# Performance work log

Measured on AMD Instinct MI355X. Metric: run time of the kernel, lower is better.

## Reference

```python
import jax, jax.numpy as jnp
import numpy as np

B, T, D = 1024, 20, 50          # batch sessions, seq len (hardcoded 20), emb dim (hardcoded 50)
S1S2 = 50 * 20                  # sample1 * sample2 friend nodes (GAT src)
DEG = 50                        # avg in-degree per dst node
E = B * DEG
NUM_USERS, NUM_ITEMS = 100000, 50000


def _lstm(x, W_ih, W_hh, b_ih, b_hh):
    """PyTorch-style LSTM (gate order i,f,g,o). x: [N,T,D] -> hs: [T,N,D]."""
    N = x.shape[0]
    h0 = jnp.zeros((N, x.shape[-1]), x.dtype)
    def step(carry, xt):
        h, c = carry
        gates = xt @ W_ih.T + h @ W_hh.T + b_ih + b_hh
        i, f, g, o = jnp.split(gates, 4, axis=-1)
        c = jax.nn.sigmoid(f) * c + jax.nn.sigmoid(i) * jnp.tanh(g)
        h = jax.nn.sigmoid(o) * jnp.tanh(c)
        return (h, c), h
    (_, _), hs = jax.lax.scan(step, (h0, h0), jnp.swapaxes(x, 0, 1))
    return hs


def _gat(feat_src, feat_dst, edge_src, edge_dst, fc_W, fc_b):
    """u_dot_v -> edge_softmax (per dst) -> u_mul_e_sum -> relu(fc)."""
    n_dst = feat_dst.shape[0]
    src_e = feat_src[edge_src]                           # [E, D] gather
    score = jnp.sum(src_e * feat_dst[edge_dst], axis=-1) # [E] u_dot_v
    m = jax.ops.segment_max(score, edge_dst, num_segments=n_dst)
    ex = jnp.exp(score - m[edge_dst])
    den = jax.ops.segment_sum(ex, edge_dst, num_segments=n_dst)
    w = ex / den[edge_dst]                               # edge_softmax
    agg = jax.ops.segment_sum(w[:, None] * src_e, edge_dst, num_segments=n_dst)
    return jax.nn.relu(agg @ fc_W.T + fc_b)


def setup_inputs() -> dict:
    key = jax.random.key(0)
    ks = jax.random.split(key, 16)
    input_session = jax.random.randint(ks[0], (B, T), 0, NUM_ITEMS, dtype=jnp.int32)
    support_nodes_layer1 = jax.random.randint(ks[1], (S1S2,), 0, NUM_USERS, dtype=jnp.int32)
    support_sessions_layer1 = jax.random.randint(ks[2], (S1S2, T), 0, NUM_ITEMS, dtype=jnp.int32)
    edge_src = jax.random.randint(ks[3], (E,), 0, S1S2, dtype=jnp.int32)
    edge_dst = jnp.repeat(jnp.arange(B, dtype=jnp.int32), DEG)  # every dst has DEG edges
    s = 0.05
    user_emb = jax.random.normal(ks[4], (NUM_USERS, D), jnp.float32) * s
    item_emb = (jax.random.normal(ks[5], (NUM_ITEMS, D), jnp.float32) * s).at[0].set(0.0)  # padding_idx=0
    W_ih = jax.random.normal(ks[6], (4 * D, D), jnp.float32) * s
    W_hh = jax.random.normal(ks[7], (4 * D, D), jnp.float32) * s
    b_ih = jax.random.normal(ks[8], (4 * D,), jnp.float32) * s
    b_hh = jax.random.normal(ks[9], (4 * D,), jnp.float32) * s
    W1 = jax.random.normal(ks[10], (D, 2 * D), jnp.float32) * s
    fc_W = jax.random.normal(ks[11], (D, D), jnp.float32) * s
    fc_b = jax.random.normal(ks[12], (D,), jnp.float32) * s
    W2 = jax.random.normal(ks[13], (D, 3 * D), jnp.float32) * s
    return {"input_session": input_session, "support_nodes_layer1": support_nodes_layer1,
            "support_sessions_layer1": support_sessions_layer1, "edge_src": edge_src,
            "edge_dst": edge_dst, "user_emb": user_emb, "item_emb": item_emb,
            "W_ih": W_ih, "W_hh": W_hh, "b_ih": b_ih, "b_hh": b_hh,
            "W1": W1, "fc_W": fc_W, "fc_b": fc_b, "W2": W2}


def reference(input_session, support_nodes_layer1, support_sessions_layer1, edge_src, edge_dst,
              user_emb, item_emb, W_ih, W_hh, b_ih, b_hh, W1, fc_W, fc_b, W2):
    # current-user short-term: LSTM over session item embeddings, take last hidden
    output = _lstm(item_emb[input_session], W_ih, W_hh, b_ih, b_hh)[-1]        # [B, D]
    # friends long-term (user emb) + short-term (LSTM over friend sessions, step 0 as in source)
    long_term1 = user_emb[support_nodes_layer1]                                 # [S1S2, D]
    short_term1 = _lstm(item_emb[support_sessions_layer1], W_ih, W_hh, b_ih, b_hh)[0]  # [S1S2, D]
    ls1 = jax.nn.relu(jnp.concatenate([long_term1, short_term1], axis=-1) @ W1.T)      # [S1S2, D]
    # GAT: gather -> per-dst edge softmax -> scatter weighted sum
    gat_out = _gat(ls1, output, edge_src, edge_dst, fc_W, fc_b)                 # [B, D]
    feat = jnp.concatenate([output, gat_out], axis=-1)                          # [B, 2D]
    sr = jnp.concatenate([output, feat], axis=-1) @ W2.T                        # [B, D]
    logits = sr @ item_emb[1:].T                                                # [B, NUM_ITEMS-1]
    return logits
```

## Files before the change

### kernel.cpp

```cpp
#include <hip/hip_runtime.h>
#include <math.h>

#define D 50
#define T 20
#define BATCH 1024
#define S1S2 1000
#define DEG 50
#define NITEMS 50000
#define NLOGITS 49999
#define KPAD 64
#define SLAB 16
#define GROUPS 8
#define GSPAN 6400
#define ITERW 256
#define NITER 25
#define NIPAD 51200
#define LSTR2 276
#define PREP_BLKS ((NIPAD * (KPAD / 2) + 255) / 256)

using bf16x8 = __attribute__((ext_vector_type(8))) __bf16;
using f32x4  = __attribute__((ext_vector_type(4))) float;

__device__ __forceinline__ float sigf(float x) { return 1.0f / (1.0f + expf(-x)); }

__device__ __forceinline__ unsigned short f2bf(float f) {
    unsigned u = __builtin_bit_cast(unsigned, f);
    u = (u + 0x7FFFu + ((u >> 16) & 1u)) >> 16;
    return (unsigned short)u;
}

__global__ __launch_bounds__(256) void fused_front_kernel(
    const int* __restrict__ sess,
    const int* __restrict__ nodes,
    const int* __restrict__ fsess,
    const float* __restrict__ user_emb,
    const float* __restrict__ item_emb,
    const float* __restrict__ W_ih,
    const float* __restrict__ W_hh,
    const float* __restrict__ b_ih,
    const float* __restrict__ b_hh,
    const float* __restrict__ W1,
    float* __restrict__ out_h,
    float* __restrict__ ls1,
    unsigned* __restrict__ item_u)
{
    const int blk = blockIdx.x;
    const int t = threadIdx.x;

    if (blk < BATCH) {
        const int b = blk;
        __shared__ float x_s[D];
        __shared__ float h_s[D];
        __shared__ float g_s[4 * D];
        __shared__ int idx_s[T];

        if (t < T) idx_s[t] = sess[b * T + t];

        float wih[D], whh[D];
        float bias = 0.f;
        if (t < 4 * D) {
            #pragma unroll
            for (int k = 0; k < D; ++k) {
                wih[k] = W_ih[t * D + k];
                whh[k] = W_hh[t * D + k];
            }
            bias = b_ih[t] + b_hh[t];
        }
        float c = 0.f;
        if (t < D) h_s[t] = 0.f;
        __syncthreads();
        if (t < D) x_s[t] = item_emb[(size_t)idx_s[0] * D + t];
        __syncthreads();

        for (int step = 0; step < T; ++step) {
            float xn = 0.f;
            if (t < D && step + 1 < T)
                xn = item_emb[(size_t)idx_s[step + 1] * D + t];
            if (t < 4 * D) {
                float g = bias;
                #pragma unroll
                for (int k = 0; k < D; ++k)
                    g += wih[k] * x_s[k] + whh[k] * h_s[k];
                g_s[t] = g;
            }
            __syncthreads();
            if (t < D) {
                float ig = sigf(g_s[t]);
                float fg = sigf(g_s[D + t]);
                float gg = tanhf(g_s[2 * D + t]);
                float og = sigf(g_s[3 * D + t]);
                c = fg * c + ig * gg;
                h_s[t] = og * tanhf(c);
                if (step + 1 < T) x_s[t] = xn;
            }
            __syncthreads();
        }
        if (t < D) out_h[b * D + t] = h_s[t];
    } else if (blk < BATCH + S1S2) {
        const int s = blk - BATCH;
        __shared__ float fx_s[D];
        __shared__ float fh_s[D];
        __shared__ float fg_s[4 * D];

        if (t < D) fx_s[t] = item_emb[(size_t)fsess[s * T] * D + t];
        __syncthreads();
        if (t < 4 * D) {
            float g = b_ih[t] + b_hh[t];
            #pragma unroll
            for (int k = 0; k < D; ++k) g += W_ih[t * D + k] * fx_s[k];
            fg_s[t] = g;
        }
        __syncthreads();
        if (t < D) {
            float ig = sigf(fg_s[t]);
            float gg = tanhf(fg_s[2 * D + t]);
            float og = sigf(fg_s[3 * D + t]);
            float c1 = ig * gg;
            fh_s[t] = og * tanhf(c1);
        }
        __syncthreads();
        if (t < D) {
            const int node = nodes[s];
            const float* ue = user_emb + (size_t)node * D;
            const float* w1r = W1 + t * 2 * D;
            float acc = 0.f;
            #pragma unroll
            for (int k = 0; k < D; ++k) acc += ue[k] * w1r[k];
            #pragma unroll
            for (int k = 0; k < D; ++k) acc += fh_s[k] * w1r[D + k];
            ls1[s * D + t] = fmaxf(acc, 0.f);
        }
    } else {
        const int idx = (blk - BATCH - S1S2) * 256 + t;
        if (idx >= NIPAD * (KPAD / 2)) return;
        const int r = idx >> 5, c2 = idx & 31;
        const int c0 = c2 * 2, c1 = c0 + 1;
        float f0 = 0.f, f1 = 0.f;
        if (r < NLOGITS) {
            const float* row = item_emb + (size_t)(1 + r) * D;
            if (c0 < D) f0 = row[c0];
            if (c1 < D) f1 = row[c1];
        }
        item_u[idx] = (unsigned)f2bf(f0) | ((unsigned)f2bf(f1) << 16);
    }
}

__global__ __launch_bounds__(64) void gat_sr_kernel(
    const float* __restrict__ out_h,
    const float* __restrict__ ls1,
    const int* __restrict__ edge_src,
    const float* __restrict__ fc_W,
    const float* __restrict__ fc_b,
    const float* __restrict__ W2,
    unsigned* __restrict__ sr_u)
{
    const int b = blockIdx.x;
    const int l = threadIdx.x;
    __shared__ float q[D];
    __shared__ int srcs[DEG];
    __shared__ float w_s[DEG];
    __shared__ float a_s[D];
    __shared__ float g_s[D];
    __shared__ float srow_s[KPAD];

    srow_s[l] = 0.f;
    if (l < D) q[l] = out_h[b * D + l];
    if (l < DEG) srcs[l] = edge_src[b * DEG + l];
    __syncthreads();

    float sc = -INFINITY;
    if (l < DEG) {
        const float* row = ls1 + (size_t)srcs[l] * D;
        float s = 0.f;
        #pragma unroll
        for (int k = 0; k < D; ++k) s += row[k] * q[k];
        sc = s;
    }
    float m = sc;
    #pragma unroll
    for (int off = 32; off; off >>= 1) m = fmaxf(m, __shfl_xor(m, off));
    float ex = (l < DEG) ? expf(sc - m) : 0.f;
    float den = ex;
    #pragma unroll
    for (int off = 32; off; off >>= 1) den += __shfl_xor(den, off);
    if (l < DEG) w_s[l] = ex / den;
    __syncthreads();

    if (l < D) {
        float a = 0.f;
        #pragma unroll
        for (int j = 0; j < DEG; ++j) a += w_s[j] * ls1[(size_t)srcs[j] * D + l];
        a_s[l] = a;
    }
    __syncthreads();
    if (l < D) {
        float g = fc_b[l];
        #pragma unroll
        for (int k = 0; k < D; ++k) g += a_s[k] * fc_W[l * D + k];
        g_s[l] = fmaxf(g, 0.f);
    }
    __syncthreads();
    if (l < D) {
        const float* w2r = W2 + l * 3 * D;
        float v = 0.f;
        #pragma unroll
        for (int k = 0; k < D; ++k) v += q[k] * (w2r[k] + w2r[D + k]);
        #pragma unroll
        for (int k = 0; k < D; ++k) v += g_s[k] * w2r[2 * D + k];
        srow_s[l] = v;
    }
    __syncthreads();
    if (l < KPAD / 2) {
        unsigned u = (unsigned)f2bf(srow_s[2 * l]) |
                     ((unsigned)f2bf(srow_s[2 * l + 1]) << 16);
        sr_u[b * (KPAD / 2) + l] = u;
    }
}

__global__ __launch_bounds__(256) void logits_mfma_kernel(
    const unsigned short* __restrict__ sr_bf,
    const unsigned short* __restrict__ item_bf,
    float* __restrict__ out)
{
    const int n = blockIdx.x;
    const int slab = n >> 3;
    const int grp  = n & 7;

    const int t = threadIdx.x;
    const int lane = t & 63;
    const int wave = t >> 6;
    const int r16 = lane & 15;
    const int g   = lane >> 4;
    const int b0 = slab * SLAB;
    const int gbase = grp * GSPAN;

    __shared__ float ls[2][SLAB * LSTR2];

    const unsigned short* bp = sr_bf + (size_t)(b0 + r16) * KPAD + g * 8;
    bf16x8 bv0 = *(const bf16x8*)(bp);
    bf16x8 bv1 = *(const bf16x8*)(bp + 32);

    auto compute = [&](int it, int buf) {
        const int ib = gbase + it * ITERW + wave * 64;
        #pragma unroll
        for (int m = 0; m < 4; ++m) {
            const unsigned short* ap =
                item_bf + (size_t)(ib + m * 16 + r16) * KPAD + g * 8;
            bf16x8 av0 = *(const bf16x8*)(ap);
            bf16x8 av1 = *(const bf16x8*)(ap + 32);
            f32x4 acc = {0.f, 0.f, 0.f, 0.f};
            acc = __builtin_amdgcn_mfma_f32_16x16x32_bf16(av0, bv0, acc, 0, 0, 0);
            acc = __builtin_amdgcn_mfma_f32_16x16x32_bf16(av1, bv1, acc, 0, 0, 0);
            *(f32x4*)&ls[buf][r16 * LSTR2 + wave * 64 + m * 16 + g * 4] = acc;
        }
    };

    compute(0, 0);
    __syncthreads();

    for (int it = 0; it < NITER; ++it) {
        const int buf = it & 1;
        const int cbase = gbase + it * ITERW;
        const int c = lane * 4;
        #pragma unroll
        for (int p = 0; p < 4; ++p) {
            const int row = wave * 4 + p;
            const f32x4 v = *(const f32x4*)&ls[buf][row * LSTR2 + c];
            float* orow = out + (size_t)(b0 + row) * NLOGITS;
            const int col = cbase + c;
            if (col + 3 < NLOGITS) {
                *(float4*)(orow + col) = make_float4(v[0], v[1], v[2], v[3]);
            } else {
                #pragma unroll
                for (int r = 0; r < 4; ++r)
                    if (col + r < NLOGITS) orow[col + r] = v[r];
            }
        }
        if (it + 1 < NITER) compute(it + 1, buf ^ 1);
        __syncthreads();
    }
}

extern "C" void kernel_launch(void* const* d_in, const int* in_sizes, int n_in,
                              void* d_out, int out_size, void* d_ws, size_t ws_size,
                              hipStream_t stream) {
    const int*   sess      = (const int*)d_in[0];
    const int*   nodes     = (const int*)d_in[1];
    const int*   fsess     = (const int*)d_in[2];
    const int*   edge_src  = (const int*)d_in[3];
    const float* user_emb  = (const float*)d_in[5];
    const float* item_emb  = (const float*)d_in[6];
    const float* W_ih      = (const float*)d_in[7];
    const float* W_hh      = (const float*)d_in[8];
    const float* b_ih      = (const float*)d_in[9];
    const float* b_hh      = (const float*)d_in[10];
    const float* W1        = (const float*)d_in[11];
    const float* fc_W      = (const float*)d_in[12];
    const float* fc_b      = (const float*)d_in[13];
    const float* W2        = (const float*)d_in[14];
    float* out = (float*)d_out;

    char* ws = (char*)d_ws;
    float*    out_h  = (float*)(ws);
    float*    ls1    = (float*)(ws + 204800);
    unsigned* sr_u   = (unsigned*)(ws + 404800);
    unsigned* item_u = (unsigned*)(ws + 535872);

    hipLaunchKernelGGL(fused_front_kernel,
                       dim3(BATCH + S1S2 + PREP_BLKS), dim3(256), 0, stream,
                       sess, nodes, fsess, user_emb, item_emb,
                       W_ih, W_hh, b_ih, b_hh, W1, out_h, ls1, item_u);
    hipLaunchKernelGGL(gat_sr_kernel, dim3(BATCH), dim3(64), 0, stream,
                       out_h, ls1, edge_src, fc_W, fc_b, W2, sr_u);
    hipLaunchKernelGGL(logits_mfma_kernel,
                       dim3(64 * GROUPS), dim3(256), 0, stream,
                       (const unsigned short*)sr_u, (const unsigned short*)item_u, out);
}
```

Baseline: 106.2 us.

## Use per-wave LDS tiles and register-prefetched item loads in logits kernel

Each wave now gets its own small LDS staging tile, which removes the block-wide __syncthreads between iterations. Item bf16 operands for the next iteration are loaded into registers before the current MFMA work, so global load latency can overlap with compute and stores. Output stores become scalar per lane (16 rows × 64 contiguous floats per wave) instead of float4 per lane, which may lower store vectorization efficiency. Register pressure goes up from holding two sets of A fragments.

```diff
diff --git a/kernel.cpp b/kernel.cpp
--- a/kernel.cpp
+++ b/kernel.cpp
@@ -15,7 +15,7 @@
 #define ITERW 256
 #define NITER 25
 #define NIPAD 51200
-#define LSTR2 276
+#define WLSTR 68
 #define PREP_BLKS ((NIPAD * (KPAD / 2) + 255) / 256)
 
 using bf16x8 = __attribute__((ext_vector_type(8))) __bf16;
@@ -234,50 +234,48 @@
     const int b0 = slab * SLAB;
     const int gbase = grp * GSPAN;
 
-    __shared__ float ls[2][SLAB * LSTR2];
+    __shared__ float ls[4][SLAB * WLSTR];
+    float* wls = &ls[wave][0];
 
     const unsigned short* bp = sr_bf + (size_t)(b0 + r16) * KPAD + g * 8;
     bf16x8 bv0 = *(const bf16x8*)(bp);
     bf16x8 bv1 = *(const bf16x8*)(bp + 32);
 
-    auto compute = [&](int it, int buf) {
+    bf16x8 a0[4], a1[4], n0[4], n1[4];
+
+    auto LOAD = [&](int it, bf16x8* v0, bf16x8* v1) {
         const int ib = gbase + it * ITERW + wave * 64;
         #pragma unroll
         for (int m = 0; m < 4; ++m) {
             const unsigned short* ap =
                 item_bf + (size_t)(ib + m * 16 + r16) * KPAD + g * 8;
-            bf16x8 av0 = *(const bf16x8*)(ap);
-            bf16x8 av1 = *(const bf16x8*)(ap + 32);
+            v0[m] = *(const bf16x8*)(ap);
+            v1[m] = *(const bf16x8*)(ap + 32);
+        }
+    };
+
+    LOAD(0, a0, a1);
+    for (int it = 0; it < NITER; ++it) {
+        if (it + 1 < NITER) LOAD(it + 1, n0, n1);
+        #pragma unroll
+        for (int m = 0; m < 4; ++m) {
             f32x4 acc = {0.f, 0.f, 0.f, 0.f};
-            acc = __builtin_amdgcn_mfma_f32_16x16x32_bf16(av0, bv0, acc, 0, 0, 0);
-            acc = __builtin_amdgcn_mfma_f32_16x16x32_bf16(av1, bv1, acc, 0, 0, 0);
-            *(f32x4*)&ls[buf][r16 * LSTR2 + wave * 64 + m * 16 + g * 4] = acc;
-        }
-    };
-
-    compute(0, 0);
-    __syncthreads();
-
-    for (int it = 0; it < NITER; ++it) {
-        const int buf = it & 1;
-        const int cbase = gbase + it * ITERW;
-        const int c = lane * 4;
-        #pragma unroll
-        for (int p = 0; p < 4; ++p) {
-            const int row = wave * 4 + p;
-            const f32x4 v = *(const f32x4*)&ls[buf][row * LSTR2 + c];
-            float* orow = out + (size_t)(b0 + row) * NLOGITS;
-            const int col = cbase + c;
-            if (col + 3 < NLOGITS) {
-                *(float4*)(orow + col) = make_float4(v[0], v[1], v[2], v[3]);
-            } else {
-                #pragma unroll
-                for (int r = 0; r < 4; ++r)
-                    if (col + r < NLOGITS) orow[col + r] = v[r];
-            }
-        }
-        if (it + 1 < NITER) compute(it + 1, buf ^ 1);
-        __syncthreads();
+            acc = __builtin_amdgcn_mfma_f32_16x16x32_bf16(a0[m], bv0, acc, 0, 0, 0);
+            acc = __builtin_amdgcn_mfma_f32_16x16x32_bf16(a1[m], bv1, acc, 0, 0, 0);
+            *(f32x4*)&wls[r16 * WLSTR + m * 16 + g * 4] = acc;
+        }
+        const int cb = gbase + it * ITERW + wave * 64;
+        const int col = cb + lane;
+        const bool ok = col < NLOGITS;
+        #pragma unroll
+        for (int p = 0; p < 16; ++p) {
+            float v = wls[p * WLSTR + lane];
+            if (ok) out[(size_t)(b0 + p) * NLOGITS + col] = v;
+        }
+        if (it + 1 < NITER) {
+            #pragma unroll
+            for (int m = 0; m < 4; ++m) { a0[m] = n0[m]; a1[m] = n1[m]; }
+        }
     }
 }
 
```

New measurement: 108.4 us. 1.02x slower.
